# Optimization experiments

Hardware: AMD Instinct MI355X
Metric: run time of the kernel (lower is better)

The kernel has to match this reference:

```python
import jax, jax.numpy as jnp
import numpy as np

DYADIC_LEVELS = 3
SIG_LEVEL = 3  # hardcoded depth-3 truncated signature (matches init_kwargs)


def path_signature(inc):
    """Truncated (level-3) path signature of a piecewise-linear path.

    inc: [..., N, d] increments. Returns [..., d + d^2 + d^3] flattened
    signature (levels 1..3, row-major tensor flattening, no scalar term),
    computed via Chen's relation: S <- S (x) exp(dx).
    """
    d = inc.shape[-1]
    bshape = inc.shape[:-2]
    inc_t = jnp.moveaxis(inc, -2, 0)  # [N, ..., d]
    s1 = jnp.zeros(bshape + (d,), inc.dtype)
    s2 = jnp.zeros(bshape + (d, d), inc.dtype)
    s3 = jnp.zeros(bshape + (d, d, d), inc.dtype)

    def step(carry, dx):
        s1, s2, s3 = carry
        dx2 = dx[..., :, None] * dx[..., None, :]          # dx (x) dx
        dx3 = dx2[..., :, :, None] * dx[..., None, None, :]
        n3 = (s3
              + s2[..., :, :, None] * dx[..., None, None, :]
              + 0.5 * s1[..., :, None, None] * dx2[..., None, :, :]
              + dx3 / 6.0)
        n2 = s2 + s1[..., :, None] * dx[..., None, :] + 0.5 * dx2
        n1 = s1 + dx
        return (n1, n2, n3), None

    (s1, s2, s3), _ = jax.lax.scan(step, (s1, s2, s3), inc_t)
    return jnp.concatenate(
        [s1, s2.reshape(bshape + (d * d,)), s3.reshape(bshape + (d * d * d,))],
        axis=-1)


def setup_inputs() -> dict:
    key = jax.random.key(0)
    x = jax.random.normal(key, (64, 1024, 64, 4), dtype=jnp.float32)
    return {"x": x}


def reference(x):
    # x: [batch, frame, element, coords] -> [batch, element, pieces, terms]
    B, T, E, D = x.shape
    xr = jnp.transpose(x, (0, 2, 1, 3))  # [B, E, T, D]
    pieces = []
    for lvl in range(DYADIC_LEVELS + 1):
        P = 2 ** lvl
        L = T // P  # frames per dyadic piece (T divisible by 2**DYADIC_LEVELS)
        xp = xr.reshape(B, E, P, L, D)
        inc = jnp.diff(xp, axis=3)  # [B, E, P, L-1, D]; signatory uses x[start:end]
        pieces.append(path_signature(inc))  # [B, E, P, terms]
    return jnp.concatenate(pieces, axis=2)  # [B, E, 15, 84]
```

## Files before the change

kernel.cpp:

```cpp
#include <hip/hip_runtime.h>

#define DEV __device__ __forceinline__


DEV void sig_step(float s1[4], float s2[16], float s3[64], const float dx[4]) {
    float w[16], u[4], g[4];
#pragma unroll
    for (int j = 0; j < 4; ++j) {
        float hj = 0.5f * dx[j];
        g[j] = s1[j] + hj;
        u[j] = fmaf(dx[j], (1.0f / 3.0f), s1[j]);
#pragma unroll
        for (int k = 0; k < 4; ++k) w[j * 4 + k] = hj * dx[k];
    }
#pragma unroll
    for (int i = 0; i < 4; ++i)
#pragma unroll
        for (int j = 0; j < 4; ++j)
#pragma unroll
            for (int k = 0; k < 4; ++k) {
                float v = s3[i * 16 + j * 4 + k];
                v = fmaf(s2[i * 4 + j], dx[k], v);
                v = fmaf(u[i], w[j * 4 + k], v);
                s3[i * 16 + j * 4 + k] = v;
            }
#pragma unroll
    for (int i = 0; i < 4; ++i)
#pragma unroll
        for (int j = 0; j < 4; ++j)
            s2[i * 4 + j] = fmaf(g[i], dx[j], s2[i * 4 + j]);
#pragma unroll
    for (int i = 0; i < 4; ++i) s1[i] += dx[i];
}

DEV void sig_init(float s1[4], float s2[16], float s3[64], const float dx[4]) {
#pragma unroll
    for (int i = 0; i < 4; ++i) s1[i] = dx[i];
#pragma unroll
    for (int j = 0; j < 4; ++j) {
        float hj = 0.5f * dx[j];
#pragma unroll
        for (int k = 0; k < 4; ++k) s2[j * 4 + k] = hj * dx[k];
    }
#pragma unroll
    for (int i = 0; i < 4; ++i) {
        float ti = dx[i] * (1.0f / 3.0f);
#pragma unroll
        for (int jk = 0; jk < 16; ++jk) s3[i * 16 + jk] = ti * s2[jk];
    }
}

DEV void chen_fold(float a1[4], float a2[16], float a3[64], const float* __restrict__ b) {
    float b1[4], b2[16];
#pragma unroll
    for (int k = 0; k < 4; ++k) b1[k] = b[k * 64];
#pragma unroll
    for (int t = 0; t < 16; ++t) b2[t] = b[(4 + t) * 64];
#pragma unroll
    for (int i = 0; i < 4; ++i)
#pragma unroll
        for (int j = 0; j < 4; ++j)
#pragma unroll
            for (int k = 0; k < 4; ++k) {
                float v = a3[i * 16 + j * 4 + k] + b[(20 + i * 16 + j * 4 + k) * 64];
                v = fmaf(a2[i * 4 + j], b1[k], v);
                v = fmaf(a1[i], b2[j * 4 + k], v);
                a3[i * 16 + j * 4 + k] = v;
            }
#pragma unroll
    for (int i = 0; i < 4; ++i)
#pragma unroll
        for (int j = 0; j < 4; ++j)
            a2[i * 4 + j] = fmaf(a1[i], b1[j], a2[i * 4 + j] + b2[i * 4 + j]);
#pragma unroll
    for (int i = 0; i < 4; ++i) a1[i] += b1[i];
}

DEV void store_sig(float* dst, const float s1[4], const float s2[16], const float s3[64]) {
#pragma unroll
    for (int t = 0; t < 4; ++t) dst[t * 64] = s1[t];
#pragma unroll
    for (int t = 0; t < 16; ++t) dst[(4 + t) * 64] = s2[t];
#pragma unroll
    for (int t = 0; t < 64; ++t) dst[(20 + t) * 64] = s3[t];
}

DEV void load_sig(const float* src, float s1[4], float s2[16], float s3[64]) {
#pragma unroll
    for (int t = 0; t < 4; ++t) s1[t] = src[t * 64];
#pragma unroll
    for (int t = 0; t < 16; ++t) s2[t] = src[(4 + t) * 64];
#pragma unroll
    for (int t = 0; t < 64; ++t) s3[t] = src[(20 + t) * 64];
}

DEV void write_out(float* ob, const float s1[4], const float s2[16], const float s3[64]) {
#pragma unroll
    for (int t = 0; t < 4; ++t) ob[t] = s1[t];
#pragma unroll
    for (int t = 0; t < 16; ++t) ob[4 + t] = s2[t];
#pragma unroll
    for (int t = 0; t < 64; ++t) ob[20 + t] = s3[t];
}

__global__ __attribute__((amdgpu_flat_work_group_size(256, 256),
                          amdgpu_waves_per_eu(2, 2)))
void piece_kernel(const float* __restrict__ x, float* __restrict__ l3sig,
                  float* __restrict__ bdxl3, float* __restrict__ out) {
    __shared__ float sigbuf[2][84][64];
    __shared__ float bdxs[4][4][64];
    const int b = blockIdx.x >> 3;
    const int p = blockIdx.x & 7;
    const int w = threadIdx.x >> 6;
    const int e = threadIdx.x & 63;
    const int c = p * 4 + w;
    const float4* xp = reinterpret_cast<const float4*>(x)
                     + (long)b * 65536 + (long)c * 32 * 64 + e;

    float4 prev = xp[0];
    if (c > 0) {
        float4 pm = xp[-64];
        float bx[4] = {prev.x - pm.x, prev.y - pm.y, prev.z - pm.z, prev.w - pm.w};
        if (w > 0) {
#pragma unroll
            for (int jj = 0; jj < 4; ++jj) bdxs[w][jj][e] = bx[jj];
        } else {
            float* bb = &bdxl3[(((long)(b * 8 + p)) * 4) * 64 + e];
#pragma unroll
            for (int jj = 0; jj < 4; ++jj) bb[jj * 64] = bx[jj];
        }
    }

    float4 buf[8];
#pragma unroll
    for (int k = 0; k < 8; ++k) buf[k] = xp[(k + 1) * 64];

    float s1[4], s2[16], s3[64];
    {
        float4 cur = buf[0];
        float dx[4] = {cur.x - prev.x, cur.y - prev.y, cur.z - prev.z, cur.w - prev.w};
        sig_init(s1, s2, s3, dx);
        prev = cur;
        buf[0] = xp[9 * 64];
    }
    for (int ii = 0; ii < 3; ++ii) {
#pragma unroll
        for (int j = 0; j < 8; ++j) {
            const int i = 2 + ii * 8 + j;
            const int slot = (i - 1) & 7;
            float4 cur = buf[slot];
            int li = i + 8; li = li > 31 ? 31 : li;
            buf[slot] = xp[li * 64];
            float dx[4] = {cur.x - prev.x, cur.y - prev.y, cur.z - prev.z, cur.w - prev.w};
            prev = cur;
            sig_step(s1, s2, s3, dx);
        }
    }
#pragma unroll
    for (int j = 0; j < 6; ++j) {
        float4 cur = buf[1 + j];
        float dx[4] = {cur.x - prev.x, cur.y - prev.y, cur.z - prev.z, cur.w - prev.w};
        prev = cur;
        sig_step(s1, s2, s3, dx);
    }

    if (w == 1 || w == 3) store_sig(&sigbuf[w >> 1][0][e], s1, s2, s3);
    __syncthreads();
    if (w == 0 || w == 2) {
        float dxl[4] = {bdxs[w + 1][0][e], bdxs[w + 1][1][e], bdxs[w + 1][2][e], bdxs[w + 1][3][e]};
        sig_step(s1, s2, s3, dxl);
        chen_fold(s1, s2, s3, &sigbuf[w >> 1][0][e]);
    }
    __syncthreads();
    if (w == 2) store_sig(&sigbuf[0][0][e], s1, s2, s3);
    __syncthreads();
    if (w == 0) {
        float dxl[4] = {bdxs[2][0][e], bdxs[2][1][e], bdxs[2][2][e], bdxs[2][3][e]};
        sig_step(s1, s2, s3, dxl);
        chen_fold(s1, s2, s3, &sigbuf[0][0][e]);
        store_sig(&l3sig[(((long)(b * 8 + p)) * 84) * 64 + e], s1, s2, s3);
        write_out(&out[(((long)(b * 64 + e)) * 15 + 7 + p) * 84], s1, s2, s3);
    }
}

__global__ __attribute__((amdgpu_flat_work_group_size(256, 256),
                          amdgpu_waves_per_eu(1, 1)))
void treeB_kernel(const float* __restrict__ l3sig, const float* __restrict__ bdxl3,
                  float* __restrict__ out) {
    __shared__ float sigbuf[2][84][64];
    const int b = blockIdx.x;
    const int w = threadIdx.x >> 6;
    const int e = threadIdx.x & 63;

    float s1[4], s2[16], s3[64];
    load_sig(&l3sig[(((long)(b * 8 + 2 * w)) * 84) * 64 + e], s1, s2, s3);
    {
        const float* bb = &bdxl3[(((long)(b * 8 + 2 * w + 1)) * 4) * 64 + e];
        float dx[4] = {bb[0], bb[64], bb[128], bb[192]};
        sig_step(s1, s2, s3, dx);
        chen_fold(s1, s2, s3, &l3sig[(((long)(b * 8 + 2 * w + 1)) * 84) * 64 + e]);
    }
    write_out(&out[(((long)(b * 64 + e)) * 15 + 3 + w) * 84], s1, s2, s3);

    if (w == 1 || w == 3) store_sig(&sigbuf[w >> 1][0][e], s1, s2, s3);
    __syncthreads();
    if (w == 0 || w == 2) {
        const int jp = (w == 0) ? 2 : 6;
        const float* bb = &bdxl3[(((long)(b * 8 + jp)) * 4) * 64 + e];
        float dx[4] = {bb[0], bb[64], bb[128], bb[192]};
        sig_step(s1, s2, s3, dx);
        chen_fold(s1, s2, s3, &sigbuf[w >> 1][0][e]);
        write_out(&out[(((long)(b * 64 + e)) * 15 + 1 + (w >> 1)) * 84], s1, s2, s3);
    }
    __syncthreads();
    if (w == 2) store_sig(&sigbuf[0][0][e], s1, s2, s3);
    __syncthreads();
    if (w == 0) {
        const float* bb = &bdxl3[(((long)(b * 8 + 4)) * 4) * 64 + e];
        float dx[4] = {bb[0], bb[64], bb[128], bb[192]};
        sig_step(s1, s2, s3, dx);
        chen_fold(s1, s2, s3, &sigbuf[0][0][e]);
        write_out(&out[(((long)(b * 64 + e)) * 15 + 0) * 84], s1, s2, s3);
    }
}

__global__ __attribute__((amdgpu_flat_work_group_size(64, 64),
                          amdgpu_waves_per_eu(1, 1)))
void direct_kernel(const float* __restrict__ x, float* __restrict__ out) {
    const int pg = blockIdx.x % 15;
    const int b = blockIdx.x / 15;
    const int e = threadIdx.x;
    int lvl, p;
    if (pg == 0)      { lvl = 0; p = 0; }
    else if (pg < 3)  { lvl = 1; p = pg - 1; }
    else if (pg < 7)  { lvl = 2; p = pg - 3; }
    else              { lvl = 3; p = pg - 7; }
    const int L = 1024 >> lvl;
    const int t0 = p * L;
    const float4* xf = reinterpret_cast<const float4*>(x);
    const long base = (long)b * 65536;

    float4 prev = xf[base + (long)t0 * 64 + e];
    float s1[4], s2[16], s3[64];
    {
        float4 cur = xf[base + (long)(t0 + 1) * 64 + e];
        float dx[4] = {cur.x - prev.x, cur.y - prev.y, cur.z - prev.z, cur.w - prev.w};
        sig_init(s1, s2, s3, dx);
        prev = cur;
    }
    for (int i = 2; i < L; ++i) {
        float4 cur = xf[base + (long)(t0 + i) * 64 + e];
        float dx[4] = {cur.x - prev.x, cur.y - prev.y, cur.z - prev.z, cur.w - prev.w};
        prev = cur;
        sig_step(s1, s2, s3, dx);
    }
    write_out(&out[(((long)(b * 64 + e)) * 15 + pg) * 84], s1, s2, s3);
}

extern "C" void kernel_launch(void* const* d_in, const int* in_sizes, int n_in,
                              void* d_out, int out_size, void* d_ws, size_t ws_size,
                              hipStream_t stream) {
    (void)in_sizes; (void)n_in; (void)out_size;
    const float* x = (const float*)d_in[0];
    float* out = (float*)d_out;

    const size_t l3_elems = (size_t)64 * 8 * 84 * 64;
    const size_t bdx_elems = (size_t)64 * 8 * 4 * 64;
    const size_t need = (l3_elems + bdx_elems) * sizeof(float);

    if (ws_size >= need) {
        float* l3sig = (float*)d_ws;
        float* bdxl3 = l3sig + l3_elems;
        piece_kernel<<<64 * 8, 256, 0, stream>>>(x, l3sig, bdxl3, out);
        treeB_kernel<<<64, 256, 0, stream>>>(l3sig, bdxl3, out);
    } else {
        direct_kernel<<<64 * 15, 64, 0, stream>>>(x, out);
    }
}
```

Measured before the change: 43.49 us.

## Split leaf stage into 64-frame halves and extend tree reduction by one level

The first kernel now processes 64-frame half-pieces (16 blocks per batch instead of 8, each wave scanning 16 frames) and stores only half-piece signatures. The level-3 output is no longer written there; the tree kernel grows to 512 threads (8 waves) and performs one extra Chen-fold level, producing levels 3 down to 0. This doubles the grid of the serial scan stage and shortens each thread's sequential chain, and it shrinks the prefetch buffer to two float4 registers to allow 3 waves per EU. In exchange it writes twice as much intermediate workspace, and the single-block-per-batch tree kernel does more serial fold work with more barriers.

Result: slower. 48.21 us (+10.9%).

```diff
diff --git a/kernel.cpp b/kernel.cpp
--- a/kernel.cpp
+++ b/kernel.cpp
@@ -104,18 +104,18 @@
 }
 
 __global__ __attribute__((amdgpu_flat_work_group_size(256, 256),
-                          amdgpu_waves_per_eu(2, 2)))
-void piece_kernel(const float* __restrict__ x, float* __restrict__ l3sig,
-                  float* __restrict__ bdxl3, float* __restrict__ out) {
+                          amdgpu_waves_per_eu(3, 3)))
+void half_kernel(const float* __restrict__ x, float* __restrict__ hsig,
+                 float* __restrict__ bdxh) {
     __shared__ float sigbuf[2][84][64];
     __shared__ float bdxs[4][4][64];
-    const int b = blockIdx.x >> 3;
-    const int p = blockIdx.x & 7;
+    const int b = blockIdx.x >> 4;
+    const int h = blockIdx.x & 15;
     const int w = threadIdx.x >> 6;
     const int e = threadIdx.x & 63;
-    const int c = p * 4 + w;
+    const int c = h * 4 + w;
     const float4* xp = reinterpret_cast<const float4*>(x)
-                     + (long)b * 65536 + (long)c * 32 * 64 + e;
+                     + (long)b * 65536 + (long)c * 16 * 64 + e;
 
     float4 prev = xp[0];
     if (c > 0) {
@@ -125,42 +125,48 @@
 #pragma unroll
             for (int jj = 0; jj < 4; ++jj) bdxs[w][jj][e] = bx[jj];
         } else {
-            float* bb = &bdxl3[(((long)(b * 8 + p)) * 4) * 64 + e];
+            float* bb = &bdxh[(((long)(b * 16 + h)) * 4) * 64 + e];
 #pragma unroll
             for (int jj = 0; jj < 4; ++jj) bb[jj * 64] = bx[jj];
         }
     }
 
-    float4 buf[8];
-#pragma unroll
-    for (int k = 0; k < 8; ++k) buf[k] = xp[(k + 1) * 64];
-
+    float4 buf0 = xp[64], buf1 = xp[2 * 64];
     float s1[4], s2[16], s3[64];
     {
-        float4 cur = buf[0];
+        float4 cur = buf0;
         float dx[4] = {cur.x - prev.x, cur.y - prev.y, cur.z - prev.z, cur.w - prev.w};
         sig_init(s1, s2, s3, dx);
         prev = cur;
-        buf[0] = xp[9 * 64];
-    }
-    for (int ii = 0; ii < 3; ++ii) {
-#pragma unroll
-        for (int j = 0; j < 8; ++j) {
-            const int i = 2 + ii * 8 + j;
-            const int slot = (i - 1) & 7;
-            float4 cur = buf[slot];
-            int li = i + 8; li = li > 31 ? 31 : li;
-            buf[slot] = xp[li * 64];
+        buf0 = xp[3 * 64];
+    }
+    for (int ii = 0; ii < 6; ++ii) {
+        {
+            const int i = 2 + 2 * ii;
+            float4 cur = buf1;
+            buf1 = xp[(i + 2) * 64];
             float dx[4] = {cur.x - prev.x, cur.y - prev.y, cur.z - prev.z, cur.w - prev.w};
             prev = cur;
             sig_step(s1, s2, s3, dx);
         }
-    }
-#pragma unroll
-    for (int j = 0; j < 6; ++j) {
-        float4 cur = buf[1 + j];
-        float dx[4] = {cur.x - prev.x, cur.y - prev.y, cur.z - prev.z, cur.w - prev.w};
-        prev = cur;
+        {
+            const int i = 3 + 2 * ii;
+            float4 cur = buf0;
+            buf0 = xp[(i + 2) * 64];
+            float dx[4] = {cur.x - prev.x, cur.y - prev.y, cur.z - prev.z, cur.w - prev.w};
+            prev = cur;
+            sig_step(s1, s2, s3, dx);
+        }
+    }
+    {
+        float4 cur = buf1;
+        float dx[4] = {cur.x - prev.x, cur.y - prev.y, cur.z - prev.z, cur.w - prev.w};
+        prev = cur;
+        sig_step(s1, s2, s3, dx);
+    }
+    {
+        float4 cur = buf0;
+        float dx[4] = {cur.x - prev.x, cur.y - prev.y, cur.z - prev.z, cur.w - prev.w};
         sig_step(s1, s2, s3, dx);
     }
 
@@ -178,48 +184,58 @@
         float dxl[4] = {bdxs[2][0][e], bdxs[2][1][e], bdxs[2][2][e], bdxs[2][3][e]};
         sig_step(s1, s2, s3, dxl);
         chen_fold(s1, s2, s3, &sigbuf[0][0][e]);
-        store_sig(&l3sig[(((long)(b * 8 + p)) * 84) * 64 + e], s1, s2, s3);
-        write_out(&out[(((long)(b * 64 + e)) * 15 + 7 + p) * 84], s1, s2, s3);
-    }
-}
-
-__global__ __attribute__((amdgpu_flat_work_group_size(256, 256),
-                          amdgpu_waves_per_eu(1, 1)))
-void treeB_kernel(const float* __restrict__ l3sig, const float* __restrict__ bdxl3,
-                  float* __restrict__ out) {
-    __shared__ float sigbuf[2][84][64];
+        store_sig(&hsig[(((long)(b * 16 + h)) * 84) * 64 + e], s1, s2, s3);
+    }
+}
+
+__global__ __attribute__((amdgpu_flat_work_group_size(512, 512),
+                          amdgpu_waves_per_eu(2, 2)))
+void tree_kernel(const float* __restrict__ hsig, const float* __restrict__ bdxh,
+                 float* __restrict__ out) {
+    __shared__ float sigbuf[4][84][64];
     const int b = blockIdx.x;
     const int w = threadIdx.x >> 6;
     const int e = threadIdx.x & 63;
 
     float s1[4], s2[16], s3[64];
-    load_sig(&l3sig[(((long)(b * 8 + 2 * w)) * 84) * 64 + e], s1, s2, s3);
-    {
-        const float* bb = &bdxl3[(((long)(b * 8 + 2 * w + 1)) * 4) * 64 + e];
-        float dx[4] = {bb[0], bb[64], bb[128], bb[192]};
-        sig_step(s1, s2, s3, dx);
-        chen_fold(s1, s2, s3, &l3sig[(((long)(b * 8 + 2 * w + 1)) * 84) * 64 + e]);
-    }
-    write_out(&out[(((long)(b * 64 + e)) * 15 + 3 + w) * 84], s1, s2, s3);
-
-    if (w == 1 || w == 3) store_sig(&sigbuf[w >> 1][0][e], s1, s2, s3);
-    __syncthreads();
-    if (w == 0 || w == 2) {
-        const int jp = (w == 0) ? 2 : 6;
-        const float* bb = &bdxl3[(((long)(b * 8 + jp)) * 4) * 64 + e];
+    load_sig(&hsig[(((long)(b * 16 + 2 * w)) * 84) * 64 + e], s1, s2, s3);
+    {
+        const float* bb = &bdxh[(((long)(b * 16 + 2 * w + 1)) * 4) * 64 + e];
+        float dx[4] = {bb[0], bb[64], bb[128], bb[192]};
+        sig_step(s1, s2, s3, dx);
+        chen_fold(s1, s2, s3, &hsig[(((long)(b * 16 + 2 * w + 1)) * 84) * 64 + e]);
+    }
+    write_out(&out[(((long)(b * 64 + e)) * 15 + 7 + w) * 84], s1, s2, s3);
+
+    if (w & 1) store_sig(&sigbuf[w >> 1][0][e], s1, s2, s3);
+    __syncthreads();
+    if (!(w & 1)) {
+        const float* bb = &bdxh[(((long)(b * 16 + 2 * w + 2)) * 4) * 64 + e];
         float dx[4] = {bb[0], bb[64], bb[128], bb[192]};
         sig_step(s1, s2, s3, dx);
         chen_fold(s1, s2, s3, &sigbuf[w >> 1][0][e]);
-        write_out(&out[(((long)(b * 64 + e)) * 15 + 1 + (w >> 1)) * 84], s1, s2, s3);
+        write_out(&out[(((long)(b * 64 + e)) * 15 + 3 + (w >> 1)) * 84], s1, s2, s3);
     }
     __syncthreads();
     if (w == 2) store_sig(&sigbuf[0][0][e], s1, s2, s3);
+    if (w == 6) store_sig(&sigbuf[1][0][e], s1, s2, s3);
+    __syncthreads();
+    if (w == 0 || w == 4) {
+        const int hh = (w == 0) ? 4 : 12;
+        const float* bb = &bdxh[(((long)(b * 16 + hh)) * 4) * 64 + e];
+        float dx[4] = {bb[0], bb[64], bb[128], bb[192]};
+        sig_step(s1, s2, s3, dx);
+        chen_fold(s1, s2, s3, &sigbuf[(w == 0) ? 0 : 1][0][e]);
+        write_out(&out[(((long)(b * 64 + e)) * 15 + 1 + (w >> 2)) * 84], s1, s2, s3);
+    }
+    __syncthreads();
+    if (w == 4) store_sig(&sigbuf[2][0][e], s1, s2, s3);
     __syncthreads();
     if (w == 0) {
-        const float* bb = &bdxl3[(((long)(b * 8 + 4)) * 4) * 64 + e];
-        float dx[4] = {bb[0], bb[64], bb[128], bb[192]};
-        sig_step(s1, s2, s3, dx);
-        chen_fold(s1, s2, s3, &sigbuf[0][0][e]);
+        const float* bb = &bdxh[(((long)(b * 16 + 8)) * 4) * 64 + e];
+        float dx[4] = {bb[0], bb[64], bb[128], bb[192]};
+        sig_step(s1, s2, s3, dx);
+        chen_fold(s1, s2, s3, &sigbuf[2][0][e]);
         write_out(&out[(((long)(b * 64 + e)) * 15 + 0) * 84], s1, s2, s3);
     }
 }
@@ -264,15 +280,15 @@
     const float* x = (const float*)d_in[0];
     float* out = (float*)d_out;
 
-    const size_t l3_elems = (size_t)64 * 8 * 84 * 64;
-    const size_t bdx_elems = (size_t)64 * 8 * 4 * 64;
-    const size_t need = (l3_elems + bdx_elems) * sizeof(float);
+    const size_t h_elems = (size_t)64 * 16 * 84 * 64;
+    const size_t bdx_elems = (size_t)64 * 16 * 4 * 64;
+    const size_t need = (h_elems + bdx_elems) * sizeof(float);
 
     if (ws_size >= need) {
-        float* l3sig = (float*)d_ws;
-        float* bdxl3 = l3sig + l3_elems;
-        piece_kernel<<<64 * 8, 256, 0, stream>>>(x, l3sig, bdxl3, out);
-        treeB_kernel<<<64, 256, 0, stream>>>(l3sig, bdxl3, out);
+        float* hsig = (float*)d_ws;
+        float* bdxh = hsig + h_elems;
+        half_kernel<<<64 * 16, 256, 0, stream>>>(x, hsig, bdxh);
+        tree_kernel<<<64, 512, 0, stream>>>(hsig, bdxh, out);
     } else {
         direct_kernel<<<64 * 15, 64, 0, stream>>>(x, out);
     }
```
